# Performance work log

Measured on AMD Instinct MI355X. Metric: run time of the kernel, lower is better.

Reference implementation:

```python
import jax, jax.numpy as jnp
import numpy as np

N = 500000   # num_nodes
B = 512      # batch_size
D = 128      # node_dim
G = 128      # global_dim
MC = 64      # max_cubes
M = 24       # max_moves_per_cube
H = 128      # MLP hidden
NEG = -1000000000.0


def setup_inputs() -> dict:
    key = jax.random.key(0)
    ks = jax.random.split(key, 8)
    node_features = jax.random.normal(ks[0], (N, D), jnp.float32)
    global_features = jax.random.normal(ks[1], (B, G), jnp.float32)
    cube_mask = jax.random.randint(ks[2], (N,), 0, 2) == 1
    batch = jnp.sort(jax.random.randint(ks[3], (N,), 0, B))
    move_mask = jax.random.randint(ks[4], (B, MC, M), 0, 2) == 1
    W1 = jax.random.normal(ks[5], (D + G, H), jnp.float32) * 0.05
    b1 = jnp.zeros((H,), jnp.float32)
    W2 = jax.random.normal(ks[6], (H, M), jnp.float32) * 0.05
    b2 = jnp.zeros((M,), jnp.float32)
    return {"node_features": node_features, "global_features": global_features,
            "W1": W1, "b1": b1, "W2": W2, "b2": b2,
            "cube_mask": cube_mask, "batch": batch, "move_mask": move_mask}


def reference(node_features, global_features, W1, b1, W2, b2, cube_mask, batch, move_mask):
    bsz = global_features.shape[0]
    max_cubes, moves = move_mask.shape[1], move_mask.shape[2]
    batch = batch.astype(jnp.int32)

    # gather global features per node, concat, small MLP (scores computed for all
    # nodes; only cube-node rows are ever scattered, matching the original math)
    combined = jnp.concatenate([node_features, global_features[batch]], axis=-1)  # [N, D+G]
    h = jax.nn.relu(combined @ W1 + b1)                                           # [N, H]
    scores = h @ W2 + b2                                                          # [N, M]

    # per-batch cumulative cube count (batch is sorted): cube_idx_in_batch
    mask_i = cube_mask.astype(jnp.int32)
    cum = jnp.cumsum(mask_i)                                   # inclusive prefix count of cubes
    counts = jax.ops.segment_sum(mask_i, batch, num_segments=bsz)
    offsets = jnp.concatenate([jnp.zeros((1,), jnp.int32),
                               jnp.cumsum(counts)[:-1].astype(jnp.int32)])
    cube_idx = cum - 1 - offsets[batch]                        # index of cube within its graph

    valid = cube_mask & (cube_idx < max_cubes)
    ib = jnp.where(valid, batch, bsz)      # out-of-range rows -> dropped
    ic = jnp.where(valid, cube_idx, 0)

    logits = jnp.full((bsz, max_cubes, moves), NEG, dtype=scores.dtype)
    logits = logits.at[ib, ic].set(scores, mode="drop")        # unique (ib, ic) per valid node

    logits_flat = logits.reshape(bsz, -1)
    logits_flat = jnp.where(move_mask.reshape(bsz, -1), logits_flat, NEG)
    return logits_flat
```

## Files before the change

kernel.cpp:

```cpp
#include <hip/hip_runtime.h>

typedef short bf16x8 __attribute__((ext_vector_type(8)));
typedef float f32x4 __attribute__((ext_vector_type(4)));

#define NEGV -1000000000.0f

__device__ __forceinline__ unsigned short f2bf(float f) {
    unsigned int u = __float_as_uint(f);
    u += 0x7FFFu + ((u >> 16) & 1u);
    return (unsigned short)(u >> 16);
}
__device__ __forceinline__ unsigned int pack2(float a, float b) {
    return (unsigned int)f2bf(a) | ((unsigned int)f2bf(b) << 16);
}

__global__ void __launch_bounds__(256, 3)
fused_kernel(const float* __restrict__ nf, const float* __restrict__ gf,
             const float* __restrict__ W1, const float* __restrict__ b1,
             const float* __restrict__ W2, const float* __restrict__ b2,
             const int* __restrict__ cube_mask, const int* __restrict__ batch,
             const int* __restrict__ move_mask, float* __restrict__ out, int N) {
    __shared__ __align__(16) char smemAB[(64 * 72 + 128 * 72) * 2];
    __shared__ __align__(16) unsigned short ldsW2[32][136];
    __shared__ int lds_node[64];
    __shared__ int wt[4];
    __shared__ unsigned long long swt[4];
    __shared__ int seg[2];
    unsigned short (*ldsA)[72]  = (unsigned short (*)[72])smemAB;
    unsigned short (*ldsB)[72]  = (unsigned short (*)[72])(smemAB + 64 * 72 * 2);
    unsigned short (*ldsH)[136] = (unsigned short (*)[136])smemAB;

    int t = threadIdx.x;
    int blk = blockIdx.x;
    int lane = t & 63, w = t >> 6;

    if (t < 64) lds_node[t] = -1;

    int w2col = t >> 3, w2k0 = (t & 7) * 16;
    float w2v[16];
#pragma unroll
    for (int j = 0; j < 16; ++j)
        w2v[j] = (w2col < 24) ? W2[(size_t)(w2k0 + j) * 24 + w2col] : 0.f;

    int wm = w >> 1, wn = w & 1;
    float b1v[4];
#pragma unroll
    for (int nt = 0; nt < 4; ++nt) b1v[nt] = b1[wn * 64 + nt * 16 + (lane & 15)];
    float b2v[2];
    int mmv[8];
#pragma unroll
    for (int ct = 0; ct < 2; ++ct) {
        int m = ct * 16 + (lane & 15);
        if (m < 24) {
            b2v[ct] = b2[m];
#pragma unroll
            for (int rr = 0; rr < 4; ++rr) {
                int row = w * 16 + (lane >> 4) * 4 + rr;
                mmv[ct * 4 + rr] = move_mask[(size_t)(blk * 64 + row) * 24 + m];
            }
        } else {
            b2v[ct] = 0.f;
#pragma unroll
            for (int rr = 0; rr < 4; ++rr) mmv[ct * 4 + rr] = 0;
        }
    }

    int kp = t >> 3, hblk = t & 7;
    float4 fW[8];
    {
        const float* s0 = W1 + (size_t)(128 + kp * 2) * 128 + hblk * 16;
#pragma unroll
        for (int i = 0; i < 4; ++i) {
            fW[i]     = *(const float4*)(s0 + i * 4);
            fW[4 + i] = *(const float4*)(s0 + 128 + i * 4);
        }
    }

    int half = t >> 7, l = t & 127;
    int target = blk + half;
    int lo = -1, hi = N;
#pragma unroll
    for (int round = 0; round < 3; ++round) {
        int span = hi - lo;
        int pos = lo + (int)(((long long)span * (l + 1)) / 129);
        int v = (pos >= 0) ? batch[pos] : -1;
        unsigned long long bal = __ballot(v >= target);
        if (lane == 0) swt[w] = bal;
        __syncthreads();
        unsigned long long mlow = swt[half * 2], mhigh = swt[half * 2 + 1];
        int j0 = mlow ? __builtin_ctzll(mlow) : (mhigh ? 64 + __builtin_ctzll(mhigh) : -1);
        if (j0 < 0) {
            lo = lo + (int)(((long long)span * 128) / 129);
        } else {
            hi = lo + (int)(((long long)span * (j0 + 1)) / 129);
            if (j0 > 0) lo = lo + (int)(((long long)span * j0) / 129);
        }
        __syncthreads();
    }
    if (l == 0) seg[half] = hi;

#pragma unroll
    for (int j = 0; j < 8; ++j)
        *(unsigned int*)&ldsW2[w2col][w2k0 + 2 * j] = pack2(w2v[2 * j], w2v[2 * j + 1]);
#pragma unroll
    for (int j = 0; j < 16; ++j) {
        float a  = ((const float*)&fW[j >> 2])[j & 3];
        float bq = ((const float*)&fW[4 + (j >> 2)])[j & 3];
        *(unsigned int*)&ldsB[hblk * 16 + j][kp * 2] = pack2(a, bq);
    }
    {
        const float* s0 = W1 + (size_t)(192 + kp * 2) * 128 + hblk * 16;
#pragma unroll
        for (int i = 0; i < 4; ++i) {
            fW[i]     = *(const float4*)(s0 + i * 4);
            fW[4 + i] = *(const float4*)(s0 + 128 + i * 4);
        }
    }
    int r = t >> 2, q = t & 3;
    float4 fG[4];
    {
        const float* srcG = gf + (size_t)blk * 128 + q * 16;
#pragma unroll
        for (int i = 0; i < 4; ++i) fG[i] = *(const float4*)(srcG + i * 4);
    }
    __syncthreads();
    int segs = seg[0], sege = seg[1];

    int found = 0;
    for (int pos = segs; pos < sege && found < 64; pos += 256) {
        int i = pos + t;
        int m = (i < sege) ? cube_mask[i] : 0;
        unsigned long long bal = __ballot(m != 0);
        int below = __popcll(bal & ((1ULL << lane) - 1ULL));
        if (lane == 0) wt[w] = __popcll(bal);
        __syncthreads();
        int waveOfs = 0, total = 0;
#pragma unroll
        for (int j = 0; j < 4; ++j) { int c = wt[j]; if (j < w) waveOfs += c; total += c; }
        int rank = found + waveOfs + below;
        if (m && rank < 64) lds_node[rank] = i;
        found += total;
        __syncthreads();
    }

    int n = lds_node[r];
    int nrow = (n >= 0) ? n : 0;
    const float* srcN = nf + (size_t)nrow * 128 + q * 16;
    float4 fN[8];
#pragma unroll
    for (int i = 0; i < 4; ++i) {
        fN[i]     = *(const float4*)(srcN + i * 4);
        fN[4 + i] = *(const float4*)(srcN + 64 + i * 4);
    }

    f32x4 acc[2][4];
#pragma unroll
    for (int i = 0; i < 2; ++i)
#pragma unroll
        for (int j = 0; j < 4; ++j) acc[i][j] = (f32x4){0.f, 0.f, 0.f, 0.f};

#define STAGE_A(s0, s1, s2, s3) do {                                             \
        unsigned short tmp[16];                                                  \
        tmp[0]  = f2bf((s0).x); tmp[1]  = f2bf((s0).y); tmp[2]  = f2bf((s0).z); tmp[3]  = f2bf((s0).w); \
        tmp[4]  = f2bf((s1).x); tmp[5]  = f2bf((s1).y); tmp[6]  = f2bf((s1).z); tmp[7]  = f2bf((s1).w); \
        tmp[8]  = f2bf((s2).x); tmp[9]  = f2bf((s2).y); tmp[10] = f2bf((s2).z); tmp[11] = f2bf((s2).w); \
        tmp[12] = f2bf((s3).x); tmp[13] = f2bf((s3).y); tmp[14] = f2bf((s3).z); tmp[15] = f2bf((s3).w); \
        *(bf16x8*)&ldsA[r][q * 16]     = *(bf16x8*)&tmp[0];                      \
        *(bf16x8*)&ldsA[r][q * 16 + 8] = *(bf16x8*)&tmp[8];                      \
    } while (0)

#define STAGE_B() do {                                                           \
        _Pragma("unroll")                                                        \
        for (int j = 0; j < 16; ++j) {                                           \
            float a_  = ((const float*)&fW[j >> 2])[j & 3];                      \
            float b_  = ((const float*)&fW[4 + (j >> 2)])[j & 3];                \
            *(unsigned int*)&ldsB[hblk * 16 + j][kp * 2] = pack2(a_, b_);        \
        }                                                                        \
    } while (0)

#define LOAD_W1(ch) do {                                                         \
        const float* s0_ = W1 + (size_t)((ch) * 64 + kp * 2) * 128 + hblk * 16;  \
        _Pragma("unroll")                                                        \
        for (int i = 0; i < 4; ++i) {                                            \
            fW[i]     = *(const float4*)(s0_ + i * 4);                           \
            fW[4 + i] = *(const float4*)(s0_ + 128 + i * 4);                     \
        }                                                                        \
    } while (0)

#define MFMA_CHUNK() do {                                                        \
        _Pragma("unroll")                                                        \
        for (int ks = 0; ks < 2; ++ks) {                                         \
            int ko = ks * 32 + (lane >> 4) * 8;                                  \
            bf16x8 af[2], bfr[4];                                                \
            _Pragma("unroll")                                                    \
            for (int mt = 0; mt < 2; ++mt)                                       \
                af[mt] = *(const bf16x8*)&ldsA[wm * 32 + mt * 16 + (lane & 15)][ko]; \
            _Pragma("unroll")                                                    \
            for (int nt = 0; nt < 4; ++nt)                                       \
                bfr[nt] = *(const bf16x8*)&ldsB[wn * 64 + nt * 16 + (lane & 15)][ko]; \
            _Pragma("unroll")                                                    \
            for (int mt = 0; mt < 2; ++mt)                                       \
                _Pragma("unroll")                                                \
                for (int nt = 0; nt < 4; ++nt)                                   \
                    acc[mt][nt] = __builtin_amdgcn_mfma_f32_16x16x32_bf16(       \
                        af[mt], bfr[nt], acc[mt][nt], 0, 0, 0);                  \
        }                                                                        \
    } while (0)

    STAGE_A(fG[0], fG[1], fG[2], fG[3]);
    __syncthreads();
    {
        const float* srcG = gf + (size_t)blk * 128 + 64 + q * 16;
#pragma unroll
        for (int i = 0; i < 4; ++i) fG[i] = *(const float4*)(srcG + i * 4);
    }
    MFMA_CHUNK();
    __syncthreads();

    STAGE_B();
    LOAD_W1(0);
    STAGE_A(fG[0], fG[1], fG[2], fG[3]);
    __syncthreads();
    MFMA_CHUNK();
    __syncthreads();

    STAGE_B();
    LOAD_W1(1);
    STAGE_A(fN[0], fN[1], fN[2], fN[3]);
    __syncthreads();
    MFMA_CHUNK();
    __syncthreads();

    STAGE_B();
    STAGE_A(fN[4], fN[5], fN[6], fN[7]);
    __syncthreads();
    MFMA_CHUNK();
    __syncthreads();

#undef STAGE_A
#undef STAGE_B
#undef LOAD_W1
#undef MFMA_CHUNK

#pragma unroll
    for (int nt = 0; nt < 4; ++nt) {
        int col = wn * 64 + nt * 16 + (lane & 15);
        float bias = b1v[nt];
#pragma unroll
        for (int mt = 0; mt < 2; ++mt) {
            int row0 = wm * 32 + mt * 16 + (lane >> 4) * 4;
#pragma unroll
            for (int rr = 0; rr < 4; ++rr) {
                float v = acc[mt][nt][rr] + bias;
                v = v > 0.f ? v : 0.f;
                ldsH[row0 + rr][col] = f2bf(v);
            }
        }
    }
    __syncthreads();

    f32x4 acc2[2];
    acc2[0] = (f32x4){0.f, 0.f, 0.f, 0.f};
    acc2[1] = (f32x4){0.f, 0.f, 0.f, 0.f};
#pragma unroll
    for (int ks = 0; ks < 4; ++ks) {
        int ko = ks * 32 + (lane >> 4) * 8;
        bf16x8 a2 = *(const bf16x8*)&ldsH[w * 16 + (lane & 15)][ko];
#pragma unroll
        for (int ct = 0; ct < 2; ++ct) {
            bf16x8 bw = *(const bf16x8*)&ldsW2[ct * 16 + (lane & 15)][ko];
            acc2[ct] = __builtin_amdgcn_mfma_f32_16x16x32_bf16(a2, bw, acc2[ct], 0, 0, 0);
        }
    }

#pragma unroll
    for (int ct = 0; ct < 2; ++ct) {
        int m = ct * 16 + (lane & 15);
        if (m >= 24) continue;
#pragma unroll
        for (int rr = 0; rr < 4; ++rr) {
            int row = w * 16 + (lane >> 4) * 4 + rr;
            size_t oidx = (size_t)(blk * 64 + row) * 24 + m;
            float v = acc2[ct][rr] + b2v[ct];
            bool keep = (lds_node[row] >= 0) && (mmv[ct * 4 + rr] != 0);
            out[oidx] = keep ? v : NEGV;
        }
    }
}

extern "C" void kernel_launch(void* const* d_in, const int* in_sizes, int n_in,
                              void* d_out, int out_size, void* d_ws, size_t ws_size,
                              hipStream_t stream) {
    const float* nf = (const float*)d_in[0];
    const float* gf = (const float*)d_in[1];
    const float* W1 = (const float*)d_in[2];
    const float* b1 = (const float*)d_in[3];
    const float* W2 = (const float*)d_in[4];
    const float* b2 = (const float*)d_in[5];
    const int* cube_mask = (const int*)d_in[6];
    const int* batch     = (const int*)d_in[7];
    const int* move_mask = (const int*)d_in[8];
    float* out = (float*)d_out;

    int N = in_sizes[6];
    int B = in_sizes[1] / 128;

    fused_kernel<<<B, 256, 0, stream>>>(nf, gf, W1, b1, W2, b2,
                                        cube_mask, batch, move_mask, out, N);
    (void)n_in; (void)out_size; (void)d_ws; (void)ws_size;
}
```

Before: 20.16 us.

## Locate batch segment via estimated window load instead of multi-round global search

```diff
diff --git a/kernel.cpp b/kernel.cpp
--- a/kernel.cpp
+++ b/kernel.cpp
@@ -4,6 +4,7 @@
 typedef float f32x4 __attribute__((ext_vector_type(4)));
 
 #define NEGV -1000000000.0f
+#define WIN 6144
 
 __device__ __forceinline__ unsigned short f2bf(float f) {
     unsigned int u = __float_as_uint(f);
@@ -19,53 +20,40 @@
              const float* __restrict__ W1, const float* __restrict__ b1,
              const float* __restrict__ W2, const float* __restrict__ b2,
              const int* __restrict__ cube_mask, const int* __restrict__ batch,
-             const int* __restrict__ move_mask, float* __restrict__ out, int N) {
+             const int* __restrict__ move_mask, float* __restrict__ out,
+             int N, int B) {
     __shared__ __align__(16) char smemAB[(64 * 72 + 128 * 72) * 2];
     __shared__ __align__(16) unsigned short ldsW2[32][136];
     __shared__ int lds_node[64];
     __shared__ int wt[4];
-    __shared__ unsigned long long swt[4];
-    __shared__ int seg[2];
+    __shared__ int seg2[2];
     unsigned short (*ldsA)[72]  = (unsigned short (*)[72])smemAB;
     unsigned short (*ldsB)[72]  = (unsigned short (*)[72])(smemAB + 64 * 72 * 2);
     unsigned short (*ldsH)[136] = (unsigned short (*)[136])smemAB;
+    int* winbuf = (int*)smemAB;
 
     int t = threadIdx.x;
     int blk = blockIdx.x;
     int lane = t & 63, w = t >> 6;
-
-    if (t < 64) lds_node[t] = -1;
-
-    int w2col = t >> 3, w2k0 = (t & 7) * 16;
-    float w2v[16];
-#pragma unroll
-    for (int j = 0; j < 16; ++j)
-        w2v[j] = (w2col < 24) ? W2[(size_t)(w2k0 + j) * 24 + w2col] : 0.f;
-
     int wm = w >> 1, wn = w & 1;
-    float b1v[4];
-#pragma unroll
-    for (int nt = 0; nt < 4; ++nt) b1v[nt] = b1[wn * 64 + nt * 16 + (lane & 15)];
-    float b2v[2];
-    int mmv[8];
-#pragma unroll
-    for (int ct = 0; ct < 2; ++ct) {
-        int m = ct * 16 + (lane & 15);
-        if (m < 24) {
-            b2v[ct] = b2[m];
-#pragma unroll
-            for (int rr = 0; rr < 4; ++rr) {
-                int row = w * 16 + (lane >> 4) * 4 + rr;
-                mmv[ct * 4 + rr] = move_mask[(size_t)(blk * 64 + row) * 24 + m];
-            }
-        } else {
-            b2v[ct] = 0.f;
-#pragma unroll
-            for (int rr = 0; rr < 4; ++rr) mmv[ct * 4 + rr] = 0;
-        }
-    }
-
+    int r = t >> 2, q = t & 3;
     int kp = t >> 3, hblk = t & 7;
+
+    long long estm = ((long long)(2 * blk + 1) * N) / (2 * B);
+    int wstart = (int)(estm - WIN / 2);
+    if (wstart < 0) wstart = 0;
+    if (wstart > N - WIN) wstart = N - WIN;
+    wstart &= ~3;
+
+    int4 wv[6];
+    {
+        const int* bsrc = batch + wstart + t * 24;
+#pragma unroll
+        for (int i = 0; i < 6; ++i) wv[i] = *(const int4*)(bsrc + i * 4);
+    }
+    int leftv = -1;
+    if (t == 0 && wstart > 0) leftv = batch[wstart - 1];
+
     float4 fW[8];
     {
         const float* s0 = W1 + (size_t)(128 + kp * 2) * 128 + hblk * 16;
@@ -75,90 +63,97 @@
             fW[4 + i] = *(const float4*)(s0 + 128 + i * 4);
         }
     }
-
-    int half = t >> 7, l = t & 127;
-    int target = blk + half;
-    int lo = -1, hi = N;
-#pragma unroll
-    for (int round = 0; round < 3; ++round) {
-        int span = hi - lo;
-        int pos = lo + (int)(((long long)span * (l + 1)) / 129);
-        int v = (pos >= 0) ? batch[pos] : -1;
-        unsigned long long bal = __ballot(v >= target);
-        if (lane == 0) swt[w] = bal;
+    float4 w2r[3];
+    {
+        const float* w2src = W2 + t * 12;
+#pragma unroll
+        for (int i = 0; i < 3; ++i) w2r[i] = *(const float4*)(w2src + i * 4);
+    }
+    float4 fG[4];
+    {
+        const float* srcG = gf + (size_t)blk * 128 + q * 16;
+#pragma unroll
+        for (int i = 0; i < 4; ++i) fG[i] = *(const float4*)(srcG + i * 4);
+    }
+    float b1v[4];
+#pragma unroll
+    for (int nt = 0; nt < 4; ++nt) b1v[nt] = b1[wn * 64 + nt * 16 + (lane & 15)];
+    float b2v[2];
+    b2v[0] = b2[lane & 15];
+    b2v[1] = ((lane & 15) < 8) ? b2[16 + (lane & 15)] : 0.f;
+
+    if (t < 64) lds_node[t] = -1;
+    if (t == 0) { seg2[0] = -1; seg2[1] = -1; }
+
+#pragma unroll
+    for (int i = 0; i < 6; ++i) *(int4*)&winbuf[4 + t * 24 + i * 4] = wv[i];
+    if (t == 0) winbuf[3] = leftv;
+#pragma unroll
+    for (int j = 0; j < 12; ++j) {
+        int f = t * 12 + j;
+        int k = f / 24, m = f - k * 24;
+        ldsW2[m][k] = f2bf(((const float*)&w2r[j >> 2])[j & 3]);
+    }
+    if (t < 128) {
+        int row = 24 + (t >> 4), c0 = (t & 15) * 8;
+        bf16x8 z; for (int i = 0; i < 8; ++i) z[i] = 0;
+        *(bf16x8*)&ldsW2[row][c0] = z;
+    }
+    __syncthreads();
+
+    {
+        int jb = t * 24;
+        int T0 = blk, T1 = blk + 1;
+#pragma unroll 4
+        for (int jj = 0; jj < 24; ++jj) {
+            int i = wstart + jb + jj;
+            int v  = winbuf[4 + jb + jj];
+            int pv = winbuf[3 + jb + jj];
+            if (v >= T0 && pv < T0) seg2[0] = i;
+            if (v >= T1 && pv < T1) seg2[1] = i;
+            if (i == N - 1) { if (v < T0) seg2[0] = N; if (v < T1) seg2[1] = N; }
+        }
+    }
+    __syncthreads();
+
+    int segs = seg2[0], sege = seg2[1];
+    if (segs < 0 || sege < 0) {
+        if (w < 2) {
+            int T = blk + w;
+            int lo = -1, hi = N;
+            for (int rd = 0; rd < 4; ++rd) {
+                long long span = hi - lo;
+                int pos = lo + (int)((span * (lane + 1)) / 65);
+                int vv = (pos <= lo) ? (-2147483647 - 1)
+                        : (pos >= hi) ? 2147483647 : batch[pos];
+                unsigned long long bal = __ballot(vv >= T);
+                if (bal) {
+                    int j0 = __builtin_ctzll(bal);
+                    int nhi = lo + (int)((span * (j0 + 1)) / 65);
+                    if (j0 > 0) lo = lo + (int)((span * j0) / 65);
+                    hi = nhi;
+                } else {
+                    lo = lo + (int)((span * 64) / 65);
+                }
+            }
+            if (lane == 0) seg2[w] = hi;
+        }
         __syncthreads();
-        unsigned long long mlow = swt[half * 2], mhigh = swt[half * 2 + 1];
-        int j0 = mlow ? __builtin_ctzll(mlow) : (mhigh ? 64 + __builtin_ctzll(mhigh) : -1);
-        if (j0 < 0) {
-            lo = lo + (int)(((long long)span * 128) / 129);
-        } else {
-            hi = lo + (int)(((long long)span * (j0 + 1)) / 129);
-            if (j0 > 0) lo = lo + (int)(((long long)span * j0) / 129);
-        }
-        __syncthreads();
-    }
-    if (l == 0) seg[half] = hi;
-
-#pragma unroll
-    for (int j = 0; j < 8; ++j)
-        *(unsigned int*)&ldsW2[w2col][w2k0 + 2 * j] = pack2(w2v[2 * j], w2v[2 * j + 1]);
-#pragma unroll
-    for (int j = 0; j < 16; ++j) {
-        float a  = ((const float*)&fW[j >> 2])[j & 3];
-        float bq = ((const float*)&fW[4 + (j >> 2)])[j & 3];
-        *(unsigned int*)&ldsB[hblk * 16 + j][kp * 2] = pack2(a, bq);
-    }
-    {
-        const float* s0 = W1 + (size_t)(192 + kp * 2) * 128 + hblk * 16;
-#pragma unroll
-        for (int i = 0; i < 4; ++i) {
-            fW[i]     = *(const float4*)(s0 + i * 4);
-            fW[4 + i] = *(const float4*)(s0 + 128 + i * 4);
-        }
-    }
-    int r = t >> 2, q = t & 3;
-    float4 fG[4];
-    {
-        const float* srcG = gf + (size_t)blk * 128 + q * 16;
-#pragma unroll
-        for (int i = 0; i < 4; ++i) fG[i] = *(const float4*)(srcG + i * 4);
-    }
-    __syncthreads();
-    int segs = seg[0], sege = seg[1];
-
-    int found = 0;
-    for (int pos = segs; pos < sege && found < 64; pos += 256) {
-        int i = pos + t;
-        int m = (i < sege) ? cube_mask[i] : 0;
-        unsigned long long bal = __ballot(m != 0);
-        int below = __popcll(bal & ((1ULL << lane) - 1ULL));
-        if (lane == 0) wt[w] = __popcll(bal);
-        __syncthreads();
-        int waveOfs = 0, total = 0;
-#pragma unroll
-        for (int j = 0; j < 4; ++j) { int c = wt[j]; if (j < w) waveOfs += c; total += c; }
-        int rank = found + waveOfs + below;
-        if (m && rank < 64) lds_node[rank] = i;
-        found += total;
-        __syncthreads();
-    }
-
-    int n = lds_node[r];
-    int nrow = (n >= 0) ? n : 0;
-    const float* srcN = nf + (size_t)nrow * 128 + q * 16;
-    float4 fN[8];
-#pragma unroll
-    for (int i = 0; i < 4; ++i) {
-        fN[i]     = *(const float4*)(srcN + i * 4);
-        fN[4 + i] = *(const float4*)(srcN + 64 + i * 4);
-    }
-
-    f32x4 acc[2][4];
-#pragma unroll
-    for (int i = 0; i < 2; ++i)
-#pragma unroll
-        for (int j = 0; j < 4; ++j) acc[i][j] = (f32x4){0.f, 0.f, 0.f, 0.f};
-
+        segs = seg2[0]; sege = seg2[1];
+    }
+
+    int base = segs & ~3;
+    if (base > N - 1024) base = (N - 1024) & ~3;
+    int4 cmv = *(const int4*)(cube_mask + base + t * 4);
+
+#define STAGE_B() do {                                                           \
+        _Pragma("unroll")                                                        \
+        for (int j = 0; j < 16; ++j) {                                           \
+            float a_ = ((const float*)&fW[j >> 2])[j & 3];                       \
+            float b_ = ((const float*)&fW[4 + (j >> 2)])[j & 3];                 \
+            *(unsigned int*)&ldsB[hblk * 16 + j][kp * 2] = pack2(a_, b_);        \
+        }                                                                        \
+    } while (0)
 #define STAGE_A(s0, s1, s2, s3) do {                                             \
         unsigned short tmp[16];                                                  \
         tmp[0]  = f2bf((s0).x); tmp[1]  = f2bf((s0).y); tmp[2]  = f2bf((s0).z); tmp[3]  = f2bf((s0).w); \
@@ -168,16 +163,6 @@
         *(bf16x8*)&ldsA[r][q * 16]     = *(bf16x8*)&tmp[0];                      \
         *(bf16x8*)&ldsA[r][q * 16 + 8] = *(bf16x8*)&tmp[8];                      \
     } while (0)
-
-#define STAGE_B() do {                                                           \
-        _Pragma("unroll")                                                        \
-        for (int j = 0; j < 16; ++j) {                                           \
-            float a_  = ((const float*)&fW[j >> 2])[j & 3];                      \
-            float b_  = ((const float*)&fW[4 + (j >> 2)])[j & 3];                \
-            *(unsigned int*)&ldsB[hblk * 16 + j][kp * 2] = pack2(a_, b_);        \
-        }                                                                        \
-    } while (0)
-
 #define LOAD_W1(ch) do {                                                         \
         const float* s0_ = W1 + (size_t)((ch) * 64 + kp * 2) * 128 + hblk * 16;  \
         _Pragma("unroll")                                                        \
@@ -186,6 +171,79 @@
             fW[4 + i] = *(const float4*)(s0_ + 128 + i * 4);                     \
         }                                                                        \
     } while (0)
+
+    STAGE_B();
+    STAGE_A(fG[0], fG[1], fG[2], fG[3]);
+    LOAD_W1(3);
+    {
+        const float* srcG = gf + (size_t)blk * 128 + 64 + q * 16;
+#pragma unroll
+        for (int i = 0; i < 4; ++i) fG[i] = *(const float4*)(srcG + i * 4);
+    }
+
+    int c_t = 0;
+#pragma unroll
+    for (int j = 0; j < 4; ++j) {
+        int i = base + t * 4 + j;
+        int mk = ((const int*)&cmv)[j];
+        c_t += (i >= segs && i < sege && mk != 0) ? 1 : 0;
+    }
+    int inc = c_t;
+#pragma unroll
+    for (int d = 1; d < 64; d <<= 1) {
+        int o = __shfl_up(inc, d);
+        if (lane >= d) inc += o;
+    }
+    if (lane == 63) wt[w] = inc;
+    __syncthreads();
+    int waveOfs = 0, total = 0;
+#pragma unroll
+    for (int j = 0; j < 4; ++j) { int c = wt[j]; if (j < w) waveOfs += c; total += c; }
+    {
+        int rank = waveOfs + (inc - c_t);
+#pragma unroll
+        for (int j = 0; j < 4; ++j) {
+            int i = base + t * 4 + j;
+            int mk = ((const int*)&cmv)[j];
+            if (i >= segs && i < sege && mk != 0) {
+                if (rank < 64) lds_node[rank] = i;
+                ++rank;
+            }
+        }
+    }
+    int found = total;
+    for (int pos = base + 1024; pos < sege && found < 64; pos += 256) {
+        int i = pos + t;
+        int mk = (i < sege) ? cube_mask[i] : 0;
+        unsigned long long bal = __ballot(mk != 0);
+        int below = __popcll(bal & ((1ULL << lane) - 1ULL));
+        if (lane == 0) wt[w] = __popcll(bal);
+        __syncthreads();
+        int wofs = 0, tot = 0;
+#pragma unroll
+        for (int j = 0; j < 4; ++j) { int c = wt[j]; if (j < w) wofs += c; tot += c; }
+        int rk = found + wofs + below;
+        if (mk && rk < 64) lds_node[rk] = i;
+        found += tot;
+        __syncthreads();
+    }
+    __syncthreads();
+
+    int n = lds_node[r];
+    int nrow = (n >= 0) ? n : 0;
+    const float* srcN = nf + (size_t)nrow * 128 + q * 16;
+    float4 fN[8];
+#pragma unroll
+    for (int i = 0; i < 4; ++i) {
+        fN[i]     = *(const float4*)(srcN + i * 4);
+        fN[4 + i] = *(const float4*)(srcN + 64 + i * 4);
+    }
+
+    f32x4 acc[2][4];
+#pragma unroll
+    for (int i = 0; i < 2; ++i)
+#pragma unroll
+        for (int j = 0; j < 4; ++j) acc[i][j] = (f32x4){0.f, 0.f, 0.f, 0.f};
 
 #define MFMA_CHUNK() do {                                                        \
         _Pragma("unroll")                                                        \
@@ -207,26 +265,30 @@
         }                                                                        \
     } while (0)
 
+    MFMA_CHUNK();
+    __syncthreads();
+
+    STAGE_B();
     STAGE_A(fG[0], fG[1], fG[2], fG[3]);
-    __syncthreads();
-    {
-        const float* srcG = gf + (size_t)blk * 128 + 64 + q * 16;
-#pragma unroll
-        for (int i = 0; i < 4; ++i) fG[i] = *(const float4*)(srcG + i * 4);
-    }
+    LOAD_W1(0);
+    __syncthreads();
     MFMA_CHUNK();
     __syncthreads();
 
     STAGE_B();
-    LOAD_W1(0);
-    STAGE_A(fG[0], fG[1], fG[2], fG[3]);
-    __syncthreads();
-    MFMA_CHUNK();
-    __syncthreads();
-
-    STAGE_B();
+    STAGE_A(fN[0], fN[1], fN[2], fN[3]);
     LOAD_W1(1);
-    STAGE_A(fN[0], fN[1], fN[2], fN[3]);
+    int mmv[8];
+#pragma unroll
+    for (int ct = 0; ct < 2; ++ct) {
+        int m = ct * 16 + (lane & 15);
+#pragma unroll
+        for (int rr = 0; rr < 4; ++rr) {
+            int row = w * 16 + (lane >> 4) * 4 + rr;
+            mmv[ct * 4 + rr] = (m < 24)
+                ? move_mask[(size_t)(blk * 64 + row) * 24 + m] : 0;
+        }
+    }
     __syncthreads();
     MFMA_CHUNK();
     __syncthreads();
@@ -306,6 +368,6 @@
     int B = in_sizes[1] / 128;
 
     fused_kernel<<<B, 256, 0, stream>>>(nf, gf, W1, b1, W2, b2,
-                                        cube_mask, batch, move_mask, out, N);
+                                        cube_mask, batch, move_mask, out, N, B);
     (void)n_in; (void)out_size; (void)d_ws; (void)ws_size;
 }
```

Result: slower. 21.24 us (+5.3%).
